# Optimization experiments

Measured on AMD Instinct MI355X. Metric: run time of the kernel, lower is better.

Reference implementation:

```python
import jax, jax.numpy as jnp
import numpy as np

V, D = 1_000_000, 128
N0, N1, N2 = 1_048_576, 131_072, 16_384
E0, E1, EP = 1_048_576, 131_072, 16_384


def setup_inputs() -> dict:
    key = jax.random.key(0)
    ks = jax.random.split(key, 20)
    inp = {
        'emb': jax.random.normal(ks[0], (V, D), jnp.float32) * 0.1,
        'bias': jnp.zeros((V, 1), jnp.float32),
        'nids': jax.random.randint(ks[1], (N0,), 0, V),
        'src0': jax.random.randint(ks[2], (E0,), 0, N0),
        'dst0': jax.random.randint(ks[3], (E0,), 0, N1),
        'w0': jax.random.uniform(ks[4], (E0,), jnp.float32),
        'src1': jax.random.randint(ks[5], (E1,), 0, N1),
        'dst1': jax.random.randint(ks[6], (E1,), 0, N2),
        'w1': jax.random.uniform(ks[7], (E1,), jnp.float32),
        'pos_src': jax.random.randint(ks[8], (EP,), 0, N2),
        'pos_dst': jax.random.randint(ks[9], (EP,), 0, N2),
        'neg_src': jax.random.randint(ks[10], (EP,), 0, N2),
        'neg_dst': jax.random.randint(ks[11], (EP,), 0, N2),
        'Q0w': jax.random.normal(ks[12], (D, D), jnp.float32) / np.sqrt(D),
        'Q0b': jnp.zeros((D,), jnp.float32),
        'W0w': jax.random.normal(ks[13], (2 * D, D), jnp.float32) / np.sqrt(2 * D),
        'W0b': jnp.zeros((D,), jnp.float32),
        'Q1w': jax.random.normal(ks[14], (D, D), jnp.float32) / np.sqrt(D),
        'Q1b': jnp.zeros((D,), jnp.float32),
        'W1w': jax.random.normal(ks[15], (2 * D, D), jnp.float32) / np.sqrt(2 * D),
        'W1b': jnp.zeros((D,), jnp.float32),
    }
    return inp


def _sage_conv(h_src, h_dst, src, dst, w, Qw, Qb, Ww, Wb, n_dst):
    # n = relu(Q h_src); m = sum_e w_e * n[src_e] per dst; ws = sum_e w_e per dst
    n = jax.nn.relu(h_src @ Qw + Qb)                                   # [N_src, H]
    m = jax.ops.segment_sum(n[src] * w[:, None], dst, num_segments=n_dst)
    ws = jnp.clip(jax.ops.segment_sum(w, dst, num_segments=n_dst), 1.0, None)[:, None]
    z = jax.nn.relu(jnp.concatenate([m / ws, h_dst], axis=1) @ Ww + Wb)
    zn = jnp.linalg.norm(z, axis=1, keepdims=True)
    return z / jnp.where(zn == 0, 1.0, zn)


def _pair_score(h, bias_nid, src, dst):
    # u_dot_v + bias_src + bias_dst  -> [E, 1]
    s = jnp.sum(h[src] * h[dst], axis=1, keepdims=True)
    return s + bias_nid[src] + bias_nid[dst]


def reference(emb, bias, nids, src0, dst0, w0, src1, dst1, w1,
              pos_src, pos_dst, neg_src, neg_dst,
              Q0w, Q0b, W0w, W0b, Q1w, Q1b, W1w, W1b):
    h = emb[nids]                                                      # [N0, D]
    h1 = _sage_conv(h, h[:N1], src0, dst0, w0, Q0w, Q0b, W0w, W0b, N1)  # [N1, D]
    h2 = _sage_conv(h1, h1[:N2], src1, dst1, w1, Q1w, Q1b, W1w, W1b, N2)  # [N2, D]
    h_item = emb[nids[:N2]] + h2                                       # [N2, D]
    bias_nid = bias[nids[:N2]]                                         # [N2, 1]
    pos = _pair_score(h_item, bias_nid, pos_src, pos_dst)
    neg = _pair_score(h_item, bias_nid, neg_src, neg_dst)
    return jax.nn.relu(neg - pos + 1.0)                                # [EP, 1]
```

## Files before the change

kernel.cpp:

```cpp
#include <hip/hip_runtime.h>
#include <stdint.h>

#define V_SZ   1000000
#define N0_SZ  1048576
#define N1_SZ  131072
#define N2_SZ  16384
#define E0_SZ  1048576
#define E1_SZ  131072
#define EP_SZ  16384

typedef short bf16x8 __attribute__((ext_vector_type(8)));
typedef float f32x4  __attribute__((ext_vector_type(4)));

__device__ __forceinline__ unsigned short f2bf(float f) {
  union { float f; unsigned u; } v; v.f = f;
  unsigned r = v.u + 0x7FFFu + ((v.u >> 16) & 1u);
  return (unsigned short)(r >> 16);
}
__device__ __forceinline__ float bf2f(unsigned short h) {
  union { unsigned u; float f; } v; v.u = ((unsigned)h) << 16;
  return v.f;
}

__global__ __launch_bounds__(256) void prepw_k(const float* __restrict__ W,
                                               unsigned short* __restrict__ WT, int K) {
  int t = blockIdx.x * 256 + threadIdx.x;
  if (t >= K * 128) return;
  int n = t & 127, k = t >> 7;
  WT[(size_t)n * K + k] = f2bf(W[t]);
}

__global__ __launch_bounds__(256) void hist_k(const int* __restrict__ dst, int E,
                                              int* __restrict__ counts) {
  int e = blockIdx.x * 256 + threadIdx.x;
  if (e < E) atomicAdd(&counts[dst[e]], 1);
}

__global__ __launch_bounds__(256) void scan_bsums_k(const int* __restrict__ counts,
                                                    int* __restrict__ bsums) {
  __shared__ int red[256];
  int base = blockIdx.x * 1024, t = threadIdx.x;
  int s = 0;
  #pragma unroll
  for (int i = 0; i < 4; i++) s += counts[base + t * 4 + i];
  red[t] = s;
  __syncthreads();
  for (int st = 128; st > 0; st >>= 1) {
    if (t < st) red[t] += red[t + st];
    __syncthreads();
  }
  if (t == 0) bsums[blockIdx.x] = red[0];
}

__global__ __launch_bounds__(256) void scan_top_k(int* __restrict__ bsums, int nb,
                                                  int* __restrict__ offs_last) {
  __shared__ int lds[256];
  int t = threadIdx.x;
  int v = (t < nb) ? bsums[t] : 0;
  lds[t] = v;
  __syncthreads();
  for (int st = 1; st < 256; st <<= 1) {
    int x = (t >= st) ? lds[t - st] : 0;
    __syncthreads();
    lds[t] += x;
    __syncthreads();
  }
  if (t < nb) bsums[t] = lds[t] - v;
  if (t == nb - 1) *offs_last = lds[t];
}

__global__ __launch_bounds__(256) void scan_final_k(const int* __restrict__ counts,
                                                    const int* __restrict__ bsums,
                                                    int* __restrict__ offs) {
  __shared__ int tsum[256];
  int base = blockIdx.x * 1024, t = threadIdx.x;
  int v0 = counts[base + t * 4 + 0], v1 = counts[base + t * 4 + 1];
  int v2 = counts[base + t * 4 + 2], v3 = counts[base + t * 4 + 3];
  int s = v0 + v1 + v2 + v3;
  tsum[t] = s;
  __syncthreads();
  for (int st = 1; st < 256; st <<= 1) {
    int x = (t >= st) ? tsum[t - st] : 0;
    __syncthreads();
    tsum[t] += x;
    __syncthreads();
  }
  int pre = bsums[blockIdx.x] + tsum[t] - s;
  offs[base + t * 4 + 0] = pre;
  offs[base + t * 4 + 1] = pre + v0;
  offs[base + t * 4 + 2] = pre + v0 + v1;
  offs[base + t * 4 + 3] = pre + v0 + v1 + v2;
}

__global__ __launch_bounds__(256) void scatter_k(const int* __restrict__ src,
                                                 const int* __restrict__ dst,
                                                 const float* __restrict__ w, int E,
                                                 const int* __restrict__ offs,
                                                 int* __restrict__ cursor,
                                                 int* __restrict__ srcs_s,
                                                 float* __restrict__ ws_s) {
  int e = blockIdx.x * 256 + threadIdx.x;
  if (e >= E) return;
  int d = dst[e];
  int p = offs[d] + atomicAdd(&cursor[d], 1);
  srcs_s[p] = src[e];
  ws_s[p] = w[e];
}

#define AM_GATHER 0
#define AM_BF16   1
#define EPI_BF16        0
#define EPI_NORM        1
#define EPI_NORM_ADDEMB 2

template <int KCHUNKS, int AM0, int AM1, int EPI>
__global__ __launch_bounds__(256) void gemm_k(const void* __restrict__ asrc0,
                                              const void* __restrict__ asrc1,
                                              const int* __restrict__ ids,
                                              const unsigned short* __restrict__ BT,
                                              const float* __restrict__ biasv,
                                              void* __restrict__ outp,
                                              const float* __restrict__ emb) {
  __shared__ unsigned short lA[64][136];
  __shared__ unsigned short lB[128][136];
  const int tid = threadIdx.x;
  const int lane = tid & 63;
  const int wid = tid >> 6;
  const int rowbase = blockIdx.x * 64;
  const int Ktot = KCHUNKS * 128;

  f32x4 acc[8];
  #pragma unroll
  for (int i = 0; i < 8; i++) acc[i] = (f32x4){0.f, 0.f, 0.f, 0.f};

  for (int c = 0; c < KCHUNKS; ++c) {
    if (c) __syncthreads();
    const int am = (c == 0) ? AM0 : AM1;
    const void* asrc = (c == 0) ? asrc0 : asrc1;
    if (am == AM_GATHER) {
      const float* fsrc = (const float*)asrc;
      #pragma unroll
      for (int i = 0; i < 8; i++) {
        int f = i * 256 + tid;
        int r = f >> 5, c4 = f & 31;
        const float* rp = fsrc + (size_t)ids[rowbase + r] * 128;
        float4 v = *(const float4*)(rp + c4 * 4);
        unsigned short* pp = &lA[r][c4 * 4];
        pp[0] = f2bf(v.x); pp[1] = f2bf(v.y); pp[2] = f2bf(v.z); pp[3] = f2bf(v.w);
      }
    } else {
      const unsigned short* bsrc = (const unsigned short*)asrc;
      #pragma unroll
      for (int i = 0; i < 4; i++) {
        int f = i * 256 + tid;
        int r = f >> 4, c8 = f & 15;
        uint4 v = *(const uint4*)(bsrc + (size_t)(rowbase + r) * 128 + c8 * 8);
        *(uint4*)(&lA[r][c8 * 8]) = v;
      }
    }
    {
      const unsigned short* bp = BT + c * 128;
      #pragma unroll
      for (int i = 0; i < 8; i++) {
        int f = i * 256 + tid;
        int n = f >> 4, c8 = f & 15;
        uint4 v = *(const uint4*)(bp + (size_t)n * Ktot + c8 * 8);
        *(uint4*)(&lB[n][c8 * 8]) = v;
      }
    }
    __syncthreads();

    const int mr = wid * 16 + (lane & 15);
    const int kq = (lane >> 4) * 8;
    #pragma unroll
    for (int kk = 0; kk < 128; kk += 32) {
      bf16x8 af = *(const bf16x8*)(&lA[mr][kk + kq]);
      #pragma unroll
      for (int nt = 0; nt < 8; ++nt) {
        bf16x8 bfr = *(const bf16x8*)(&lB[nt * 16 + (lane & 15)][kk + kq]);
        acc[nt] = __builtin_amdgcn_mfma_f32_16x16x32_bf16(af, bfr, acc[nt], 0, 0, 0);
      }
    }
  }

  const int crow = wid * 16 + ((lane >> 4) << 2);
  float vreg[8][4];
  #pragma unroll
  for (int nt = 0; nt < 8; ++nt) {
    int col = nt * 16 + (lane & 15);
    float b = biasv[col];
    #pragma unroll
    for (int r = 0; r < 4; ++r) {
      float v = acc[nt][r] + b;
      vreg[nt][r] = v > 0.f ? v : 0.f;
    }
  }
  if (EPI == EPI_BF16) {
    unsigned short* op = (unsigned short*)outp;
    #pragma unroll
    for (int nt = 0; nt < 8; ++nt) {
      int col = nt * 16 + (lane & 15);
      #pragma unroll
      for (int r = 0; r < 4; ++r)
        op[(size_t)(rowbase + crow + r) * 128 + col] = f2bf(vreg[nt][r]);
    }
  } else {
    float ss[4] = {0.f, 0.f, 0.f, 0.f};
    #pragma unroll
    for (int nt = 0; nt < 8; ++nt)
      #pragma unroll
      for (int r = 0; r < 4; ++r) ss[r] += vreg[nt][r] * vreg[nt][r];
    #pragma unroll
    for (int r = 0; r < 4; ++r) {
      ss[r] += __shfl_xor(ss[r], 1);
      ss[r] += __shfl_xor(ss[r], 2);
      ss[r] += __shfl_xor(ss[r], 4);
      ss[r] += __shfl_xor(ss[r], 8);
    }
    float sc[4];
    #pragma unroll
    for (int r = 0; r < 4; ++r) sc[r] = ss[r] > 0.f ? rsqrtf(ss[r]) : 1.0f;
    if (EPI == EPI_NORM) {
      unsigned short* op = (unsigned short*)outp;
      #pragma unroll
      for (int nt = 0; nt < 8; ++nt) {
        int col = nt * 16 + (lane & 15);
        #pragma unroll
        for (int r = 0; r < 4; ++r)
          op[(size_t)(rowbase + crow + r) * 128 + col] = f2bf(vreg[nt][r] * sc[r]);
      }
    } else {
      float* op = (float*)outp;
      #pragma unroll
      for (int nt = 0; nt < 8; ++nt) {
        int col = nt * 16 + (lane & 15);
        #pragma unroll
        for (int r = 0; r < 4; ++r) {
          int row = rowbase + crow + r;
          op[(size_t)row * 128 + col] =
              vreg[nt][r] * sc[r] + emb[(size_t)ids[row] * 128 + col];
        }
      }
    }
  }
}

__global__ __launch_bounds__(256) void agg_k(const unsigned short* __restrict__ nsrc,
                                             const int* __restrict__ offs,
                                             const int* __restrict__ srcs_s,
                                             const float* __restrict__ ws_s,
                                             unsigned short* __restrict__ aout, int ndst) {
  int wid = threadIdx.x >> 6, lane = threadIdx.x & 63;
  int d = blockIdx.x * 4 + wid;
  if (d >= ndst) return;
  int beg = offs[d], end = offs[d + 1];
  float ax = 0.f, ay = 0.f, wsum = 0.f;
  for (int j = beg; j < end; ++j) {
    int s = srcs_s[j];
    float w = ws_s[j];
    unsigned u = *(const unsigned*)(nsrc + (size_t)s * 128 + lane * 2);
    ax += w * bf2f((unsigned short)(u & 0xffff));
    ay += w * bf2f((unsigned short)(u >> 16));
    wsum += w;
  }
  float inv = 1.0f / fmaxf(wsum, 1.0f);
  unsigned o = ((unsigned)f2bf(ay * inv) << 16) | (unsigned)f2bf(ax * inv);
  *(unsigned*)(aout + (size_t)d * 128 + lane * 2) = o;
}

__global__ __launch_bounds__(256) void gatherbias_k(const float* __restrict__ bias,
                                                    const int* __restrict__ nids,
                                                    float* __restrict__ biasg) {
  int i = blockIdx.x * 256 + threadIdx.x;
  if (i < N2_SZ) biasg[i] = bias[nids[i]];
}

__global__ __launch_bounds__(256) void score_k(const float* __restrict__ hitem,
                                               const float* __restrict__ biasg,
                                               const int* __restrict__ ps,
                                               const int* __restrict__ pd,
                                               const int* __restrict__ ns,
                                               const int* __restrict__ nd,
                                               float* __restrict__ out) {
  int wid = threadIdx.x >> 6, lane = threadIdx.x & 63;
  int e = blockIdx.x * 4 + wid;
  if (e >= EP_SZ) return;
  int a = ps[e], b = pd[e], c = ns[e], d = nd[e];
  float2 va = ((const float2*)(hitem + (size_t)a * 128))[lane];
  float2 vb = ((const float2*)(hitem + (size_t)b * 128))[lane];
  float2 vc = ((const float2*)(hitem + (size_t)c * 128))[lane];
  float2 vd = ((const float2*)(hitem + (size_t)d * 128))[lane];
  float dp = va.x * vb.x + va.y * vb.y;
  float dn = vc.x * vd.x + vc.y * vd.y;
  #pragma unroll
  for (int m = 1; m < 64; m <<= 1) {
    dp += __shfl_xor(dp, m);
    dn += __shfl_xor(dn, m);
  }
  if (lane == 0) {
    float sp = dp + biasg[a] + biasg[b];
    float sn = dn + biasg[c] + biasg[d];
    out[e] = fmaxf(sn - sp + 1.0f, 0.0f);
  }
}

extern "C" void kernel_launch(void* const* d_in, const int* in_sizes, int n_in,
                              void* d_out, int out_size, void* d_ws, size_t ws_size,
                              hipStream_t stream) {
  const float* emb  = (const float*)d_in[0];
  const float* bias = (const float*)d_in[1];
  const int* nids   = (const int*)d_in[2];
  const int* src0   = (const int*)d_in[3];
  const int* dst0   = (const int*)d_in[4];
  const float* w0   = (const float*)d_in[5];
  const int* src1   = (const int*)d_in[6];
  const int* dst1   = (const int*)d_in[7];
  const float* w1   = (const float*)d_in[8];
  const int* pos_src = (const int*)d_in[9];
  const int* pos_dst = (const int*)d_in[10];
  const int* neg_src = (const int*)d_in[11];
  const int* neg_dst = (const int*)d_in[12];
  const float* Q0w = (const float*)d_in[13];
  const float* Q0b = (const float*)d_in[14];
  const float* W0w = (const float*)d_in[15];
  const float* W0b = (const float*)d_in[16];
  const float* Q1w = (const float*)d_in[17];
  const float* Q1b = (const float*)d_in[18];
  const float* W1w = (const float*)d_in[19];
  const float* W1b = (const float*)d_in[20];
  float* out = (float*)d_out;

  char* ws = (char*)d_ws;
  size_t p = 0;
  auto carve = [&](size_t sz) { void* r = ws + p; p = (p + sz + 255) & ~(size_t)255; return r; };

  unsigned short* n0 = (unsigned short*)carve((size_t)N0_SZ * 128 * 2);
  unsigned short* h1    = (unsigned short*)(ws + 0);
  unsigned short* n1    = (unsigned short*)(ws + 33554432);
  unsigned short* a1    = (unsigned short*)(ws + 67108864);
  float*          hitem = (float*)(ws + 71303168);
  float*          biasg = (float*)(ws + 79691776);

  unsigned short* a0  = (unsigned short*)carve((size_t)N1_SZ * 128 * 2);
  unsigned short* Q0T = (unsigned short*)carve(128 * 128 * 2);
  unsigned short* W0T = (unsigned short*)carve(256 * 128 * 2);
  unsigned short* Q1T = (unsigned short*)carve(128 * 128 * 2);
  unsigned short* W1T = (unsigned short*)carve(256 * 128 * 2);
  int*   counts0 = (int*)carve(N1_SZ * 4);
  int*   offs0   = (int*)carve((N1_SZ + 1) * 4);
  int*   cursor0 = (int*)carve(N1_SZ * 4);
  int*   srcs_s0 = (int*)carve(E0_SZ * 4);
  float* ws_s0   = (float*)carve(E0_SZ * 4);
  int*   counts1 = (int*)carve(N2_SZ * 4);
  int*   offs1   = (int*)carve((N2_SZ + 1) * 4);
  int*   cursor1 = (int*)carve(N2_SZ * 4);
  int*   srcs_s1 = (int*)carve(E1_SZ * 4);
  float* ws_s1   = (float*)carve(E1_SZ * 4);
  int*   bsums0  = (int*)carve(128 * 4);
  int*   bsums1  = (int*)carve(16 * 4);
  (void)ws_size; (void)in_sizes; (void)n_in; (void)out_size;

  hipMemsetAsync(counts0, 0, N1_SZ * 4, stream);
  hipMemsetAsync(cursor0, 0, N1_SZ * 4, stream);
  hipMemsetAsync(counts1, 0, N2_SZ * 4, stream);
  hipMemsetAsync(cursor1, 0, N2_SZ * 4, stream);

  prepw_k<<<64, 256, 0, stream>>>(Q0w, Q0T, 128);
  prepw_k<<<128, 256, 0, stream>>>(W0w, W0T, 256);
  prepw_k<<<64, 256, 0, stream>>>(Q1w, Q1T, 128);
  prepw_k<<<128, 256, 0, stream>>>(W1w, W1T, 256);

  hist_k<<<E0_SZ / 256, 256, 0, stream>>>(dst0, E0_SZ, counts0);
  scan_bsums_k<<<N1_SZ / 1024, 256, 0, stream>>>(counts0, bsums0);
  scan_top_k<<<1, 256, 0, stream>>>(bsums0, N1_SZ / 1024, offs0 + N1_SZ);
  scan_final_k<<<N1_SZ / 1024, 256, 0, stream>>>(counts0, bsums0, offs0);
  scatter_k<<<E0_SZ / 256, 256, 0, stream>>>(src0, dst0, w0, E0_SZ, offs0, cursor0, srcs_s0, ws_s0);
  hist_k<<<E1_SZ / 256, 256, 0, stream>>>(dst1, E1_SZ, counts1);
  scan_bsums_k<<<N2_SZ / 1024, 256, 0, stream>>>(counts1, bsums1);
  scan_top_k<<<1, 256, 0, stream>>>(bsums1, N2_SZ / 1024, offs1 + N2_SZ);
  scan_final_k<<<N2_SZ / 1024, 256, 0, stream>>>(counts1, bsums1, offs1);
  scatter_k<<<E1_SZ / 256, 256, 0, stream>>>(src1, dst1, w1, E1_SZ, offs1, cursor1, srcs_s1, ws_s1);

  gemm_k<1, AM_GATHER, AM_GATHER, EPI_BF16>
      <<<N0_SZ / 64, 256, 0, stream>>>(emb, nullptr, nids, Q0T, Q0b, n0, nullptr);
  agg_k<<<N1_SZ / 4, 256, 0, stream>>>(n0, offs0, srcs_s0, ws_s0, a0, N1_SZ);
  gemm_k<2, AM_BF16, AM_GATHER, EPI_NORM>
      <<<N1_SZ / 64, 256, 0, stream>>>(a0, emb, nids, W0T, W0b, h1, nullptr);
  gemm_k<1, AM_BF16, AM_BF16, EPI_BF16>
      <<<N1_SZ / 64, 256, 0, stream>>>(h1, nullptr, nullptr, Q1T, Q1b, n1, nullptr);
  agg_k<<<N2_SZ / 4, 256, 0, stream>>>(n1, offs1, srcs_s1, ws_s1, a1, N2_SZ);
  gemm_k<2, AM_BF16, AM_BF16, EPI_NORM_ADDEMB>
      <<<N2_SZ / 64, 256, 0, stream>>>(a1, h1, nids, W1T, W1b, hitem, emb);

  gatherbias_k<<<N2_SZ / 256, 256, 0, stream>>>(bias, nids, biasg);
  score_k<<<EP_SZ / 4, 256, 0, stream>>>(hitem, biasg, pos_src, pos_dst,
                                         neg_src, neg_dst, out);
}
```

Measured before the change: 1.167 ms.

## Merge preprocessing launches, batch agg edge loads via shuffles, pack bf16 stores

Merges the per-layer weight transpose, histogram, scan and scatter kernels into combined launches over concatenated count/cursor buffers, and folds the four memsets into one. Drops the separate bias-gather kernel by having the scoring kernel read bias through nids directly. The aggregation kernel now loads up to 64 edge indices and weights cooperatively per wavefront, broadcasts them with shuffles and unrolls four row gathers for more memory-level parallelism. The gather path of the GEMM packs bf16 pairs into one 8-byte LDS store. The aim is to cut launch overhead and latency-bound serial gathers, at the cost of more complex index logic.

```diff
diff --git a/kernel.cpp b/kernel.cpp
--- a/kernel.cpp
+++ b/kernel.cpp
@@ -21,19 +21,32 @@
   union { unsigned u; float f; } v; v.u = ((unsigned)h) << 16;
   return v.f;
 }
-
-__global__ __launch_bounds__(256) void prepw_k(const float* __restrict__ W,
-                                               unsigned short* __restrict__ WT, int K) {
+__device__ __forceinline__ unsigned pack2bf(float a, float b) {
+  return ((unsigned)f2bf(b) << 16) | (unsigned)f2bf(a);
+}
+
+__global__ __launch_bounds__(256) void prepw_all_k(
+    const float* __restrict__ Q0w, const float* __restrict__ W0w,
+    const float* __restrict__ Q1w, const float* __restrict__ W1w,
+    unsigned short* __restrict__ Q0T, unsigned short* __restrict__ W0T,
+    unsigned short* __restrict__ Q1T, unsigned short* __restrict__ W1T) {
   int t = blockIdx.x * 256 + threadIdx.x;
-  if (t >= K * 128) return;
-  int n = t & 127, k = t >> 7;
-  WT[(size_t)n * K + k] = f2bf(W[t]);
-}
-
-__global__ __launch_bounds__(256) void hist_k(const int* __restrict__ dst, int E,
-                                              int* __restrict__ counts) {
+  const float* W; unsigned short* WT; int K; int base;
+  if (t < 16384)      { W = Q0w; WT = Q0T; K = 128; base = 0; }
+  else if (t < 49152) { W = W0w; WT = W0T; K = 256; base = 16384; }
+  else if (t < 65536) { W = Q1w; WT = Q1T; K = 128; base = 49152; }
+  else                { W = W1w; WT = W1T; K = 256; base = 65536; }
+  int u = t - base;
+  int n = u & 127, k = u >> 7;
+  WT[(size_t)n * K + k] = f2bf(W[u]);
+}
+
+__global__ __launch_bounds__(256) void hist_all_k(const int* __restrict__ dst0,
+                                                  const int* __restrict__ dst1,
+                                                  int* __restrict__ counts) {
   int e = blockIdx.x * 256 + threadIdx.x;
-  if (e < E) atomicAdd(&counts[dst[e]], 1);
+  if (e < E0_SZ) atomicAdd(&counts[dst0[e]], 1);
+  else if (e < E0_SZ + E1_SZ) atomicAdd(&counts[N1_SZ + dst1[e - E0_SZ]], 1);
 }
 
 __global__ __launch_bounds__(256) void scan_bsums_k(const int* __restrict__ counts,
@@ -52,11 +65,14 @@
   if (t == 0) bsums[blockIdx.x] = red[0];
 }
 
-__global__ __launch_bounds__(256) void scan_top_k(int* __restrict__ bsums, int nb,
-                                                  int* __restrict__ offs_last) {
+__global__ __launch_bounds__(256) void scan_top2_k(int* __restrict__ bsums,
+                                                   int* __restrict__ offs0_last,
+                                                   int* __restrict__ offs1_last) {
   __shared__ int lds[256];
-  int t = threadIdx.x;
-  int v = (t < nb) ? bsums[t] : 0;
+  int b = blockIdx.x, t = threadIdx.x;
+  int nb = (b == 0) ? 128 : 16;
+  int off = (b == 0) ? 0 : 128;
+  int v = (t < nb) ? bsums[off + t] : 0;
   lds[t] = v;
   __syncthreads();
   for (int st = 1; st < 256; st <<= 1) {
@@ -65,15 +81,17 @@
     lds[t] += x;
     __syncthreads();
   }
-  if (t < nb) bsums[t] = lds[t] - v;
-  if (t == nb - 1) *offs_last = lds[t];
+  if (t < nb) bsums[off + t] = lds[t] - v;
+  if (t == nb - 1) *((b == 0) ? offs0_last : offs1_last) = lds[t];
 }
 
 __global__ __launch_bounds__(256) void scan_final_k(const int* __restrict__ counts,
                                                     const int* __restrict__ bsums,
-                                                    int* __restrict__ offs) {
+                                                    int* __restrict__ offs0,
+                                                    int* __restrict__ offs1) {
   __shared__ int tsum[256];
-  int base = blockIdx.x * 1024, t = threadIdx.x;
+  int b = blockIdx.x, t = threadIdx.x;
+  int base = b * 1024;
   int v0 = counts[base + t * 4 + 0], v1 = counts[base + t * 4 + 1];
   int v2 = counts[base + t * 4 + 2], v3 = counts[base + t * 4 + 3];
   int s = v0 + v1 + v2 + v3;
@@ -85,26 +103,34 @@
     tsum[t] += x;
     __syncthreads();
   }
-  int pre = bsums[blockIdx.x] + tsum[t] - s;
-  offs[base + t * 4 + 0] = pre;
-  offs[base + t * 4 + 1] = pre + v0;
-  offs[base + t * 4 + 2] = pre + v0 + v1;
-  offs[base + t * 4 + 3] = pre + v0 + v1 + v2;
-}
-
-__global__ __launch_bounds__(256) void scatter_k(const int* __restrict__ src,
-                                                 const int* __restrict__ dst,
-                                                 const float* __restrict__ w, int E,
-                                                 const int* __restrict__ offs,
-                                                 int* __restrict__ cursor,
-                                                 int* __restrict__ srcs_s,
-                                                 float* __restrict__ ws_s) {
+  int pre = bsums[b] + tsum[t] - s;
+  int* op = (b < 128) ? (offs0 + base) : (offs1 + base - N1_SZ);
+  op[t * 4 + 0] = pre;
+  op[t * 4 + 1] = pre + v0;
+  op[t * 4 + 2] = pre + v0 + v1;
+  op[t * 4 + 3] = pre + v0 + v1 + v2;
+}
+
+__global__ __launch_bounds__(256) void scatter_all_k(
+    const int* __restrict__ src0, const int* __restrict__ dst0, const float* __restrict__ w0,
+    const int* __restrict__ src1, const int* __restrict__ dst1, const float* __restrict__ w1,
+    const int* __restrict__ offs0, const int* __restrict__ offs1,
+    int* __restrict__ cursor,
+    int* __restrict__ srcs_s0, float* __restrict__ ws_s0,
+    int* __restrict__ srcs_s1, float* __restrict__ ws_s1) {
   int e = blockIdx.x * 256 + threadIdx.x;
-  if (e >= E) return;
-  int d = dst[e];
-  int p = offs[d] + atomicAdd(&cursor[d], 1);
-  srcs_s[p] = src[e];
-  ws_s[p] = w[e];
+  if (e < E0_SZ) {
+    int d = dst0[e];
+    int p = offs0[d] + atomicAdd(&cursor[d], 1);
+    srcs_s0[p] = src0[e];
+    ws_s0[p] = w0[e];
+  } else if (e < E0_SZ + E1_SZ) {
+    int ee = e - E0_SZ;
+    int d = dst1[ee];
+    int p = offs1[d] + atomicAdd(&cursor[N1_SZ + d], 1);
+    srcs_s1[p] = src1[ee];
+    ws_s1[p] = w1[ee];
+  }
 }
 
 #define AM_GATHER 0
@@ -145,8 +171,10 @@
         int r = f >> 5, c4 = f & 31;
         const float* rp = fsrc + (size_t)ids[rowbase + r] * 128;
         float4 v = *(const float4*)(rp + c4 * 4);
-        unsigned short* pp = &lA[r][c4 * 4];
-        pp[0] = f2bf(v.x); pp[1] = f2bf(v.y); pp[2] = f2bf(v.z); pp[3] = f2bf(v.w);
+        uint2 pk;
+        pk.x = pack2bf(v.x, v.y);
+        pk.y = pack2bf(v.z, v.w);
+        *(uint2*)(&lA[r][c4 * 4]) = pk;
       }
     } else {
       const unsigned short* bsrc = (const unsigned short*)asrc;
@@ -255,28 +283,47 @@
   if (d >= ndst) return;
   int beg = offs[d], end = offs[d + 1];
   float ax = 0.f, ay = 0.f, wsum = 0.f;
-  for (int j = beg; j < end; ++j) {
-    int s = srcs_s[j];
-    float w = ws_s[j];
-    unsigned u = *(const unsigned*)(nsrc + (size_t)s * 128 + lane * 2);
-    ax += w * bf2f((unsigned short)(u & 0xffff));
-    ay += w * bf2f((unsigned short)(u >> 16));
-    wsum += w;
+  for (int base = beg; base < end; base += 64) {
+    int cnt = min(64, end - base);
+    int sv = 0; float wv = 0.f;
+    if (lane < cnt) { sv = srcs_s[base + lane]; wv = ws_s[base + lane]; }
+    int j = 0;
+    for (; j + 4 <= cnt; j += 4) {
+      int s0 = __shfl(sv, j),     s1 = __shfl(sv, j + 1);
+      int s2 = __shfl(sv, j + 2), s3 = __shfl(sv, j + 3);
+      float w0 = __shfl(wv, j),     w1 = __shfl(wv, j + 1);
+      float w2 = __shfl(wv, j + 2), w3 = __shfl(wv, j + 3);
+      unsigned u0 = *(const unsigned*)(nsrc + (size_t)s0 * 128 + lane * 2);
+      unsigned u1 = *(const unsigned*)(nsrc + (size_t)s1 * 128 + lane * 2);
+      unsigned u2 = *(const unsigned*)(nsrc + (size_t)s2 * 128 + lane * 2);
+      unsigned u3 = *(const unsigned*)(nsrc + (size_t)s3 * 128 + lane * 2);
+      ax += w0 * bf2f((unsigned short)(u0 & 0xffff));
+      ay += w0 * bf2f((unsigned short)(u0 >> 16));
+      ax += w1 * bf2f((unsigned short)(u1 & 0xffff));
+      ay += w1 * bf2f((unsigned short)(u1 >> 16));
+      ax += w2 * bf2f((unsigned short)(u2 & 0xffff));
+      ay += w2 * bf2f((unsigned short)(u2 >> 16));
+      ax += w3 * bf2f((unsigned short)(u3 & 0xffff));
+      ay += w3 * bf2f((unsigned short)(u3 >> 16));
+      wsum += w0 + w1 + w2 + w3;
+    }
+    for (; j < cnt; ++j) {
+      int s = __shfl(sv, j);
+      float w = __shfl(wv, j);
+      unsigned u = *(const unsigned*)(nsrc + (size_t)s * 128 + lane * 2);
+      ax += w * bf2f((unsigned short)(u & 0xffff));
+      ay += w * bf2f((unsigned short)(u >> 16));
+      wsum += w;
+    }
   }
   float inv = 1.0f / fmaxf(wsum, 1.0f);
   unsigned o = ((unsigned)f2bf(ay * inv) << 16) | (unsigned)f2bf(ax * inv);
   *(unsigned*)(aout + (size_t)d * 128 + lane * 2) = o;
 }
 
-__global__ __launch_bounds__(256) void gatherbias_k(const float* __restrict__ bias,
-                                                    const int* __restrict__ nids,
-                                                    float* __restrict__ biasg) {
-  int i = blockIdx.x * 256 + threadIdx.x;
-  if (i < N2_SZ) biasg[i] = bias[nids[i]];
-}
-
 __global__ __launch_bounds__(256) void score_k(const float* __restrict__ hitem,
-                                               const float* __restrict__ biasg,
+                                               const float* __restrict__ bias,
+                                               const int* __restrict__ nids,
                                                const int* __restrict__ ps,
                                                const int* __restrict__ pd,
                                                const int* __restrict__ ns,
@@ -298,8 +345,8 @@
     dn += __shfl_xor(dn, m);
   }
   if (lane == 0) {
-    float sp = dp + biasg[a] + biasg[b];
-    float sn = dn + biasg[c] + biasg[d];
+    float sp = dp + bias[nids[a]] + bias[nids[b]];
+    float sn = dn + bias[nids[c]] + bias[nids[d]];
     out[e] = fmaxf(sn - sp + 1.0f, 0.0f);
   }
 }
@@ -339,47 +386,35 @@
   unsigned short* n1    = (unsigned short*)(ws + 33554432);
   unsigned short* a1    = (unsigned short*)(ws + 67108864);
   float*          hitem = (float*)(ws + 71303168);
-  float*          biasg = (float*)(ws + 79691776);
 
   unsigned short* a0  = (unsigned short*)carve((size_t)N1_SZ * 128 * 2);
   unsigned short* Q0T = (unsigned short*)carve(128 * 128 * 2);
   unsigned short* W0T = (unsigned short*)carve(256 * 128 * 2);
   unsigned short* Q1T = (unsigned short*)carve(128 * 128 * 2);
   unsigned short* W1T = (unsigned short*)carve(256 * 128 * 2);
-  int*   counts0 = (int*)carve(N1_SZ * 4);
+  int* cnt_all = (int*)carve((size_t)(N1_SZ + N2_SZ) * 2 * 4);
+  int* counts  = cnt_all;
+  int* cursor  = cnt_all + (N1_SZ + N2_SZ);
   int*   offs0   = (int*)carve((N1_SZ + 1) * 4);
-  int*   cursor0 = (int*)carve(N1_SZ * 4);
+  int*   offs1   = (int*)carve((N2_SZ + 1) * 4);
   int*   srcs_s0 = (int*)carve(E0_SZ * 4);
   float* ws_s0   = (float*)carve(E0_SZ * 4);
-  int*   counts1 = (int*)carve(N2_SZ * 4);
-  int*   offs1   = (int*)carve((N2_SZ + 1) * 4);
-  int*   cursor1 = (int*)carve(N2_SZ * 4);
   int*   srcs_s1 = (int*)carve(E1_SZ * 4);
   float* ws_s1   = (float*)carve(E1_SZ * 4);
-  int*   bsums0  = (int*)carve(128 * 4);
-  int*   bsums1  = (int*)carve(16 * 4);
+  int*   bsums   = (int*)carve(160 * 4);
   (void)ws_size; (void)in_sizes; (void)n_in; (void)out_size;
 
-  hipMemsetAsync(counts0, 0, N1_SZ * 4, stream);
-  hipMemsetAsync(cursor0, 0, N1_SZ * 4, stream);
-  hipMemsetAsync(counts1, 0, N2_SZ * 4, stream);
-  hipMemsetAsync(cursor1, 0, N2_SZ * 4, stream);
-
-  prepw_k<<<64, 256, 0, stream>>>(Q0w, Q0T, 128);
-  prepw_k<<<128, 256, 0, stream>>>(W0w, W0T, 256);
-  prepw_k<<<64, 256, 0, stream>>>(Q1w, Q1T, 128);
-  prepw_k<<<128, 256, 0, stream>>>(W1w, W1T, 256);
-
-  hist_k<<<E0_SZ / 256, 256, 0, stream>>>(dst0, E0_SZ, counts0);
-  scan_bsums_k<<<N1_SZ / 1024, 256, 0, stream>>>(counts0, bsums0);
-  scan_top_k<<<1, 256, 0, stream>>>(bsums0, N1_SZ / 1024, offs0 + N1_SZ);
-  scan_final_k<<<N1_SZ / 1024, 256, 0, stream>>>(counts0, bsums0, offs0);
-  scatter_k<<<E0_SZ / 256, 256, 0, stream>>>(src0, dst0, w0, E0_SZ, offs0, cursor0, srcs_s0, ws_s0);
-  hist_k<<<E1_SZ / 256, 256, 0, stream>>>(dst1, E1_SZ, counts1);
-  scan_bsums_k<<<N2_SZ / 1024, 256, 0, stream>>>(counts1, bsums1);
-  scan_top_k<<<1, 256, 0, stream>>>(bsums1, N2_SZ / 1024, offs1 + N2_SZ);
-  scan_final_k<<<N2_SZ / 1024, 256, 0, stream>>>(counts1, bsums1, offs1);
-  scatter_k<<<E1_SZ / 256, 256, 0, stream>>>(src1, dst1, w1, E1_SZ, offs1, cursor1, srcs_s1, ws_s1);
+  hipMemsetAsync(cnt_all, 0, (size_t)(N1_SZ + N2_SZ) * 2 * 4, stream);
+
+  prepw_all_k<<<384, 256, 0, stream>>>(Q0w, W0w, Q1w, W1w, Q0T, W0T, Q1T, W1T);
+
+  hist_all_k<<<(E0_SZ + E1_SZ) / 256, 256, 0, stream>>>(dst0, dst1, counts);
+  scan_bsums_k<<<(N1_SZ + N2_SZ) / 1024, 256, 0, stream>>>(counts, bsums);
+  scan_top2_k<<<2, 256, 0, stream>>>(bsums, offs0 + N1_SZ, offs1 + N2_SZ);
+  scan_final_k<<<(N1_SZ + N2_SZ) / 1024, 256, 0, stream>>>(counts, bsums, offs0, offs1);
+  scatter_all_k<<<(E0_SZ + E1_SZ) / 256, 256, 0, stream>>>(
+      src0, dst0, w0, src1, dst1, w1, offs0, offs1, cursor,
+      srcs_s0, ws_s0, srcs_s1, ws_s1);
 
   gemm_k<1, AM_GATHER, AM_GATHER, EPI_BF16>
       <<<N0_SZ / 64, 256, 0, stream>>>(emb, nullptr, nids, Q0T, Q0b, n0, nullptr);
@@ -392,7 +427,6 @@
   gemm_k<2, AM_BF16, AM_BF16, EPI_NORM_ADDEMB>
       <<<N2_SZ / 64, 256, 0, stream>>>(a1, h1, nids, W1T, W1b, hitem, emb);
 
-  gatherbias_k<<<N2_SZ / 256, 256, 0, stream>>>(bias, nids, biasg);
-  score_k<<<EP_SZ / 4, 256, 0, stream>>>(hitem, biasg, pos_src, pos_dst,
+  score_k<<<EP_SZ / 4, 256, 0, stream>>>(hitem, bias, nids, pos_src, pos_dst,
                                          neg_src, neg_dst, out);
 }
```

Measured after the change: 1.041 ms. 1.12x faster.
